# Performance work log

Measured on AMD Instinct MI355X. Metric: run time of the kernel, lower is better.

## Reference

```python
import jax, jax.numpy as jnp
import numpy as np

B = 8192         # graphs per batch
NPG = 39         # nodes per graph (from 4560 = 40*(105+9))
N = B * NPG      # total nodes
DEG = 8          # avg degree
E = N * DEG      # total edges
NEG_SLOPE = 0.2


def _glorot(key, shape):
    fan = sum(shape) if len(shape) > 1 else shape[0] + 1
    s = jnp.sqrt(6.0 / fan)
    return jax.random.uniform(key, shape, jnp.float32, -s, s)


def setup_inputs() -> dict:
    key = jax.random.key(0)
    ks = jax.random.split(key, 32)
    x = jax.random.normal(ks[0], (N, 1), jnp.float32)
    # edges constrained within each graph
    epg = NPG * DEG
    off = jnp.repeat(jnp.arange(B, dtype=jnp.int64) * NPG, epg)
    src = jax.random.randint(ks[1], (B * epg,), 0, NPG, jnp.int64) + off
    dst = jax.random.randint(ks[2], (B * epg,), 0, NPG, jnp.int64) + off
    edge_index = jnp.stack([src, dst], 0)
    batch_ids = jnp.repeat(jnp.arange(B, dtype=jnp.int64), NPG)
    dims = [(1, 8), (8, 64), (64, 32), (32, 9)]
    p = {}
    ki = 3
    for li, (fi, fo) in enumerate(dims, 1):
        p[f'W{li}'] = _glorot(ks[ki], (fi, fo)); ki += 1
        p[f'as{li}'] = _glorot(ks[ki], (fo,)); ki += 1
        p[f'ad{li}'] = _glorot(ks[ki], (fo,)); ki += 1
        p[f'b{li}'] = jnp.zeros((fo,), jnp.float32)
    p['lw1'] = _glorot(ks[ki], (4560, 1024)); ki += 1
    p['lb1'] = jnp.zeros((1024,), jnp.float32)
    p['lw2'] = _glorot(ks[ki], (1024, 128)); ki += 1
    p['lb2'] = jnp.zeros((128,), jnp.float32)
    p['lw3'] = _glorot(ks[ki], (128, 9)); ki += 1
    p['lb3'] = jnp.zeros((9,), jnp.float32)
    return {'x': x, 'edge_index': edge_index, 'batch_ids': batch_ids, **p}


def gat_layer(x, src, dst, W, a_s, a_d, b):
    # PyG GATConv, heads=1: h=xW; e_ij = LeakyReLU(a_s.h[src]+a_d.h[dst]);
    # softmax per destination node; out = sum_j alpha * h[src] + bias
    h = x @ W                                   # [N, Fo]
    s_n = h @ a_s                               # [N]
    d_n = h @ a_d                               # [N]
    e = jax.nn.leaky_relu(s_n[src] + d_n[dst], NEG_SLOPE)   # [E+N]
    m = jax.ops.segment_max(e, dst, num_segments=N)
    w = jnp.exp(e - m[dst])
    denom = jax.ops.segment_sum(w, dst, num_segments=N)
    alpha = w / (denom[dst] + 1e-16)
    out = jax.ops.segment_sum(h[src] * alpha[:, None], dst, num_segments=N)
    return out + b


def reference(x, edge_index, batch_ids, W1, as1, ad1, b1, W2, as2, ad2, b2,
              W3, as3, ad3, b3, W4, as4, ad4, b4, lw1, lb1, lw2, lb2, lw3, lb3):
    # add self-loops (PyG GATConv default)
    sl = jnp.arange(N, dtype=edge_index.dtype)
    src = jnp.concatenate([edge_index[0], sl])
    dst = jnp.concatenate([edge_index[1], sl])
    pool = lambda h: jax.ops.segment_max(h, batch_ids, num_segments=B)

    x0 = x.reshape(-1, 1)
    res = x0.reshape(B, -1)
    out0 = pool(x0)
    h1 = jax.nn.relu(gat_layer(x0, src, dst, W1, as1, ad1, b1))
    res1, out1 = h1.reshape(B, -1), pool(h1)
    h2 = jax.nn.relu(gat_layer(h1, src, dst, W2, as2, ad2, b2))
    res2, out2 = h2.reshape(B, -1), pool(h2)
    h3 = jax.nn.relu(gat_layer(h2, src, dst, W3, as3, ad3, b3))
    res3, out3 = h3.reshape(B, -1), pool(h3)
    h4 = jax.nn.relu(gat_layer(h3, src, dst, W4, as4, ad4, b4))
    res4, out4 = h4.reshape(B, -1), pool(h4)

    f = jnp.concatenate([res, res1, res2, res3, res4,
                         out0, out1, out2, out3, out4], axis=1)  # [B, 4560]
    f = jax.nn.relu(f @ lw1 + lb1)
    f = jax.nn.relu(f @ lw2 + lb2)
    return f @ lw3 + lb3
```

## Files before the change

kernel.cpp:

```cpp
#include <hip/hip_runtime.h>

#define NPG   39
#define NGRAPH 8192
#define EPG   312
#define EDG   351
#define E0    2555904
#define FDIM  4560
#define KP    4608

typedef __bf16 bf16x8 __attribute__((ext_vector_type(8)));
typedef float  f32x4  __attribute__((ext_vector_type(4)));

__device__ __forceinline__ unsigned short f2b(float f) {
  unsigned int u = __float_as_uint(f);
  u += 0x7fffu + ((u >> 16) & 1u);
  return (unsigned short)(u >> 16);
}
__device__ __forceinline__ unsigned int pk2(float lo, float hi) {
  return (unsigned int)f2b(lo) | ((unsigned int)f2b(hi) << 16);
}
__device__ __forceinline__ float b2f(unsigned short u) {
  return __uint_as_float((unsigned int)u << 16);
}
__device__ __forceinline__ void wsync() {
  asm volatile("s_waitcnt lgkmcnt(0)" ::: "memory");
}
__device__ __forceinline__ void gsync() {
  asm volatile("s_waitcnt vmcnt(0) lgkmcnt(0)" ::: "memory");
}

__shared__ alignas(16) unsigned short Htb[32 * 64];
__shared__ alignas(16) unsigned short alf16[40 * 64];
__shared__ float sn[40];
__shared__ float dn[48];
__shared__ unsigned char csr_src[EDG + 1];
__shared__ unsigned short csr_ptr[NPG + 1];

template<int Fi, int Fo, int KPAD, int KT1, int NT_STORE, int HALVES,
         int DT, int SCOL, int DCOL>
__device__ __forceinline__ void layerM(float x0,
                                       const unsigned short* __restrict__ Wb,
                                       const float* __restrict__ W1,
                                       const float* __restrict__ as1,
                                       const float* __restrict__ ad1,
                                       const float* __restrict__ bias,
                                       unsigned short* __restrict__ f_row,
                                       int in_off, int res_off, int out_off,
                                       int lane) {
  constexpr int NTH = NT_STORE / HALVES;
  constexpr int VW  = (HALVES == 2) ? 32 : Fo;
  constexpr bool SWZST = (VW == 32);
  const int r15 = lane & 15, g = lane >> 4;
  const f32x4 z = {0.f, 0.f, 0.f, 0.f};
  const uint4 z4 = {0u, 0u, 0u, 0u};
  unsigned short* stg = Htb;

#pragma unroll
  for (int i = 0; i < 5; ++i) *(uint4*)&alf16[lane * 8 + i * 512] = z4;

  if constexpr (Fi == 1) {
    float was = 0.f, wad = 0.f;
#pragma unroll
    for (int o = 0; o < 8; ++o) { float w = W1[o]; was += w * as1[o]; wad += w * ad1[o]; }
    if (lane < NPG) {
      sn[lane] = x0 * was; dn[lane] = x0 * wad;
#pragma unroll
      for (int o = 0; o < 8; ++o) {
        int idx = o * 64 + ((((lane >> 3) ^ (o & 7)) << 3)) + (lane & 7);
        Htb[idx] = f2b(x0 * W1[o]);
      }
    }
  } else {
    gsync();
    f32x4 cd[3];
#pragma unroll
    for (int mt = 0; mt < 3; ++mt) cd[mt] = z;
#pragma unroll
    for (int kt = 0; kt < KT1; ++kt) {
      bf16x8 aF[3];
#pragma unroll
      for (int mt = 0; mt < 3; ++mt) {
        int row = 16 * mt + r15;
        row = (row > 39) ? 39 : row;
        aF[mt] = *(const bf16x8*)&f_row[in_off + row * Fi + kt * 32 + g * 8];
      }
      bf16x8 bD = *(const bf16x8*)&Wb[(16 * DT + r15) * KPAD + kt * 32 + g * 8];
#pragma unroll
      for (int mt = 0; mt < 3; ++mt)
        cd[mt] = __builtin_amdgcn_mfma_f32_16x16x32_bf16(aF[mt], bD, cd[mt], 0, 0, 0);
    }
#pragma unroll
    for (int mt = 0; mt < 3; ++mt)
#pragma unroll
      for (int v = 0; v < 4; ++v) {
        float t = cd[mt][v] + __shfl_xor(cd[mt][v], 4);
        int r = 16 * mt + g * 4 + v;
        if (r15 == SCOL && r < NPG) sn[r] = t;
        if (r15 == DCOL && r < NPG) dn[r] = t;
      }
  }
  wsync();

  if (lane < NPG) {
    int rs = csr_ptr[lane], re = csr_ptr[lane + 1];
    float dv = dn[lane];
    float m = -3.4e38f;
    for (int k = rs; k < re; ++k) {
      float e = sn[csr_src[k]] + dv;
      e = (e >= 0.f) ? e : 0.2f * e;
      m = fmaxf(m, e);
    }
    float den = 0.f;
    for (int k = rs; k < re; ++k) {
      int s = csr_src[k];
      float e = sn[s] + dv;
      e = (e >= 0.f) ? e : 0.2f * e;
      float w = __expf(e - m);
      int idx = lane * 64 + ((((s >> 3) ^ (lane & 7)) << 3)) + (s & 7);
      float cur = b2f(alf16[idx]);
      unsigned short nb = f2b(cur + w);
      alf16[idx] = nb;
      den += b2f(nb) - cur;
    }
    dn[lane] = 1.f / (den + 1e-16f);
  }
  wsync();

  float invr[3][4];
#pragma unroll
  for (int mt = 0; mt < 3; ++mt)
#pragma unroll
    for (int v = 0; v < 4; ++v) invr[mt][v] = dn[16 * mt + g * 4 + v];

  float pool_[NT_STORE];
#pragma unroll
  for (int s = 0; s < NT_STORE; ++s) pool_[s] = 0.f;

#pragma unroll
  for (int h = 0; h < HALVES; ++h) {
    const int colbase = (HALVES == 2) ? 32 * h : 0;
    if constexpr (Fi > 1) {
      f32x4 c1[3][NTH];
#pragma unroll
      for (int mt = 0; mt < 3; ++mt)
#pragma unroll
        for (int tl = 0; tl < NTH; ++tl) c1[mt][tl] = z;
#pragma unroll
      for (int kt = 0; kt < KT1; ++kt) {
        bf16x8 aF[3];
#pragma unroll
        for (int mt = 0; mt < 3; ++mt) {
          int row = 16 * mt + r15;
          row = (row > 39) ? 39 : row;
          aF[mt] = *(const bf16x8*)&f_row[in_off + row * Fi + kt * 32 + g * 8];
        }
#pragma unroll
        for (int tl = 0; tl < NTH; ++tl) {
          int nt = h * NTH + tl;
          bf16x8 bW = *(const bf16x8*)&Wb[(16 * nt + r15) * KPAD + kt * 32 + g * 8];
#pragma unroll
          for (int mt = 0; mt < 3; ++mt)
            c1[mt][tl] = __builtin_amdgcn_mfma_f32_16x16x32_bf16(aF[mt], bW, c1[mt][tl], 0, 0, 0);
        }
      }
#pragma unroll
      for (int tl = 0; tl < NTH; ++tl) {
        int p = r15 + 16 * tl;
#pragma unroll
        for (int mt = 0; mt < 3; ++mt) {
          uint2 w;
          w.x = pk2(c1[mt][tl][0], c1[mt][tl][1]);
          w.y = pk2(c1[mt][tl][2], c1[mt][tl][3]);
          int idx = p * 64 + (((2 * mt + (g >> 1)) ^ (p & 7)) << 3) + (g & 1) * 4;
          *(uint2*)&Htb[idx] = w;
        }
      }
    }
    wsync();
    f32x4 c2[3][NTH];
#pragma unroll
    for (int mt = 0; mt < 3; ++mt)
#pragma unroll
      for (int tl = 0; tl < NTH; ++tl) c2[mt][tl] = z;
#pragma unroll
    for (int kt = 0; kt < 2; ++kt) {
      bf16x8 aA[3];
#pragma unroll
      for (int mt = 0; mt < 3; ++mt) {
        int row = 16 * mt + r15;
        aA[mt] = *(const bf16x8*)&alf16[row * 64 + ((((4 * kt + g) ^ (row & 7))) << 3)];
      }
#pragma unroll
      for (int tl = 0; tl < NTH; ++tl) {
        int p = r15 + 16 * tl;
        bf16x8 bH = *(const bf16x8*)&Htb[p * 64 + ((((4 * kt + g) ^ (p & 7))) << 3)];
#pragma unroll
        for (int mt = 0; mt < 3; ++mt)
          c2[mt][tl] = __builtin_amdgcn_mfma_f32_16x16x32_bf16(aA[mt], bH, c2[mt][tl], 0, 0, 0);
      }
    }
#pragma unroll
    for (int tl = 0; tl < NTH; ++tl) {
      int c = r15 + 16 * (h * NTH + tl);
      float bv = (c < Fo) ? bias[c] : 0.f;
#pragma unroll
      for (int mt = 0; mt < 3; ++mt)
#pragma unroll
        for (int v = 0; v < 4; ++v) {
          int r = 16 * mt + g * 4 + v;
          float val = fmaxf(c2[mt][tl][v] * invr[mt][v] + bv, 0.f);
          if (r < NPG && c < Fo) {
            int sc = c - colbase;
            int so = SWZST ? ((sc >> 3) ^ ((r >> 2) & 3)) : (sc >> 3);
            stg[r * VW + (so << 3) + (sc & 7)] = f2b(val);
            pool_[h * NTH + tl] = fmaxf(pool_[h * NTH + tl], val);
          }
        }
    }
    wsync();

    if constexpr (Fo == 9) {
      for (int j = lane; j < 43; j += 64)
        *(uint4*)&f_row[res_off + j * 8] = *(const uint4*)&stg[j * 8];
      if (lane < 7) f_row[res_off + 344 + lane] = stg[344 + lane];
    } else {
      constexpr int OPR = VW / 8;
      for (int j = lane; j < NPG * OPR; j += 64) {
        int r = (OPR == 4) ? (j >> 2) : j;
        int o = (OPR == 4) ? (j & 3) : 0;
        int so = SWZST ? (o ^ ((r >> 2) & 3)) : o;
        *(uint4*)&f_row[res_off + r * Fo + colbase + 8 * o] =
            *(const uint4*)&stg[r * VW + 8 * so];
      }
    }
    wsync();
  }

#pragma unroll
  for (int s = 0; s < NT_STORE; ++s) {
    float pv = pool_[s];
    pv = fmaxf(pv, __shfl_xor(pv, 16));
    pv = fmaxf(pv, __shfl_xor(pv, 32));
    int c = r15 + 16 * s;
    if (g == 0 && c < Fo) f_row[out_off + c] = f2b(pv);
  }
}

__global__ __launch_bounds__(64, 4) void gat_fused(
    const float* __restrict__ x, const int* __restrict__ ei,
    const float* __restrict__ W1, const float* __restrict__ as1, const float* __restrict__ ad1,
    const float* __restrict__ b1, const float* __restrict__ b2,
    const float* __restrict__ b3, const float* __restrict__ b4,
    const unsigned short* __restrict__ Wb,
    unsigned short* __restrict__ f) {
  const int b = blockIdx.x;
  const int lane = threadIdx.x;
  const int base = b * NPG;
  const int* srcg = ei + (size_t)b * EPG;
  const int* dstg = ei + E0 + (size_t)b * EPG;
  unsigned short* f_row = f + (size_t)b * KP;
  int* cnt = (int*)sn;
  const uint4 z4 = {0u, 0u, 0u, 0u};

#pragma unroll
  for (int i = 0; i < 4; ++i) *(uint4*)&Htb[lane * 8 + i * 512] = z4;

  float xv = 0.f;
  if (lane < NPG) {
    xv = x[(size_t)base + lane];
    f_row[lane] = f2b(xv);
  }
  if (lane == 0) f_row[39] = 0;
  if (lane < KP - 4561) f_row[4561 + lane] = 0;
  float mx = (lane < NPG) ? xv : -3.4e38f;
#pragma unroll
  for (int st = 1; st < 64; st <<= 1) { float t = __shfl_xor(mx, st); mx = fmaxf(mx, t); }
  if (lane == 0) f_row[4447] = f2b(mx);
  if (lane < NPG) cnt[lane] = 1;
  wsync();

  int es[5], ed[5];
#pragma unroll
  for (int it = 0; it < 5; ++it) {
    int e = lane + 64 * it;
    if (e < EPG) {
      int s = srcg[e] - base, d = dstg[e] - base;
      s = min(max(s, 0), NPG - 1);
      d = min(max(d, 0), NPG - 1);
      es[it] = s; ed[it] = d;
      atomicAdd(&cnt[d], 1);
    } else { es[it] = -1; ed[it] = 0; }
  }
  wsync();

  int c = (lane < NPG) ? cnt[lane] : 0;
  int v = c;
#pragma unroll
  for (int off = 1; off < 64; off <<= 1) { int t = __shfl_up(v, off); if (lane >= off) v += t; }
  int excl = v - c;
  if (lane < NPG) csr_ptr[lane] = (unsigned short)excl;
  if (lane == NPG - 1) csr_ptr[NPG] = (unsigned short)EDG;
  wsync();
  if (lane < NPG) cnt[lane] = excl;
  wsync();

  if (lane < NPG) { int p = atomicAdd(&cnt[lane], 1); csr_src[p] = (unsigned char)lane; }
#pragma unroll
  for (int it = 0; it < 5; ++it) {
    if (es[it] >= 0) {
      int p = atomicAdd(&cnt[ed[it]], 1);
      p = min(p, EDG - 1);
      csr_src[p] = (unsigned char)es[it];
    }
  }
  wsync();

  const unsigned short* Wb2 = Wb;
  const unsigned short* Wb3 = Wb + 2560;
  const unsigned short* Wb4 = Wb + 5632;

  layerM< 1,  8,  0,  0,  1,  1,  0,  0,  0>(xv, nullptr, W1, as1, ad1, b1, f_row, 0,    40,   4448, lane);
  layerM< 8, 64, 32,  1,  4,  2,  4,  0,  1>(0.f, Wb2, nullptr, nullptr, nullptr, b2, f_row, 40,   352,  4456, lane);
  layerM<64, 32, 64,  2,  2,  1,  2,  0,  1>(0.f, Wb3, nullptr, nullptr, nullptr, b3, f_row, 352,  2848, 4520, lane);
  layerM<32,  9, 32,  1,  1,  1,  0, 10, 11>(0.f, Wb4, nullptr, nullptr, nullptr, b4, f_row, 2848, 4096, 4552, lane);
}

__global__ __launch_bounds__(256) void prep_wb(
    const float* __restrict__ W2, const float* __restrict__ as2, const float* __restrict__ ad2,
    const float* __restrict__ W3, const float* __restrict__ as3, const float* __restrict__ ad3,
    const float* __restrict__ W4, const float* __restrict__ as4, const float* __restrict__ ad4,
    unsigned short* __restrict__ Wb) {
  const int tid = threadIdx.x;
  for (int i = tid; i < 80 * 32; i += 256) {
    int o = i >> 5, k = i & 31; float v = 0.f;
    if (k < 8) {
      if (o < 64) v = W2[k * 64 + o];
      else if (o == 64 || o == 68) { float s = 0; for (int j = 0; j < 64; ++j) s += W2[k * 64 + j] * as2[j];
        float hi = b2f(f2b(s)); v = (o == 64) ? hi : (s - hi); }
      else if (o == 65 || o == 69) { float s = 0; for (int j = 0; j < 64; ++j) s += W2[k * 64 + j] * ad2[j];
        float hi = b2f(f2b(s)); v = (o == 65) ? hi : (s - hi); }
    }
    Wb[i] = f2b(v);
  }
  for (int i = tid; i < 48 * 64; i += 256) {
    int o = i >> 6, k = i & 63; float v = 0.f;
    if (o < 32) v = W3[k * 32 + o];
    else if (o == 32 || o == 36) { float s = 0; for (int j = 0; j < 32; ++j) s += W3[k * 32 + j] * as3[j];
      float hi = b2f(f2b(s)); v = (o == 32) ? hi : (s - hi); }
    else if (o == 33 || o == 37) { float s = 0; for (int j = 0; j < 32; ++j) s += W3[k * 32 + j] * ad3[j];
      float hi = b2f(f2b(s)); v = (o == 33) ? hi : (s - hi); }
    Wb[2560 + i] = f2b(v);
  }
  for (int i = tid; i < 16 * 32; i += 256) {
    int o = i >> 5, k = i & 31; float v = 0.f;
    if (o < 9) v = W4[k * 9 + o];
    else if (o == 10 || o == 14) { float s = 0; for (int j = 0; j < 9; ++j) s += W4[k * 9 + j] * as4[j];
      float hi = b2f(f2b(s)); v = (o == 10) ? hi : (s - hi); }
    else if (o == 11 || o == 15) { float s = 0; for (int j = 0; j < 9; ++j) s += W4[k * 9 + j] * ad4[j];
      float hi = b2f(f2b(s)); v = (o == 11) ? hi : (s - hi); }
    Wb[5632 + i] = f2b(v);
  }
}

template<bool PERM>
__global__ __launch_bounds__(256) void tcast(const float* __restrict__ in,
                                             unsigned short* __restrict__ out,
                                             int K, int NN, int Kpad) {
  __shared__ float tile[64 * 65];
  const int k0 = blockIdx.x * 64, n0 = blockIdx.y * 64;
  const int tid = threadIdx.x;
#pragma unroll
  for (int i = 0; i < 16; ++i) {
    int idx = i * 256 + tid;
    int r = idx >> 6, c = idx & 63;
    int k = k0 + r;
    int ko;
    if constexpr (PERM) {
      ko = (k < 39) ? k : ((k == 39 || k > FDIM) ? -1 : k - 1);
    } else {
      ko = (k < K) ? k : -1;
    }
    tile[r * 65 + c] = (ko >= 0) ? in[(size_t)ko * NN + n0 + c] : 0.f;
  }
  __syncthreads();
#pragma unroll
  for (int i = 0; i < 16; ++i) {
    int idx = i * 256 + tid;
    int r = idx >> 6, c = idx & 63;
    out[(size_t)(n0 + r) * Kpad + k0 + c] = f2b(tile[c * 65 + r]);
  }
}

template<bool OUT_BF16>
__global__ __launch_bounds__(256) void mfma_gemm(const unsigned short* __restrict__ A,
    const unsigned short* __restrict__ Bt, unsigned short* __restrict__ Cb,
    float* __restrict__ Cf, const float* __restrict__ bias, int K, int N, int gridN) {
  __shared__ alignas(16) unsigned short As[128 * 64];
  __shared__ alignas(16) unsigned short Bs[128 * 64];
  const int tid = threadIdx.x;
  const int lane = tid & 63;
  const int wave = tid >> 6;
  const int wy = wave >> 1, wx = wave & 1;

  const int wg = blockIdx.x;
  const int xcd = wg & 7, idx = wg >> 3;
  const int mpr = (int)(gridDim.x >> 3) / gridN;
  const int m_local = idx / gridN;
  const int n = idx - m_local * gridN;
  const int m0 = (xcd * mpr + m_local) * 128;
  const int n0 = n * 128;

  f32x4 acc[4][4];
  const f32x4 z = {0.f, 0.f, 0.f, 0.f};
#pragma unroll
  for (int i = 0; i < 4; ++i)
#pragma unroll
    for (int j = 0; j < 4; ++j) acc[i][j] = z;

  const int srow = lane >> 3;
  const int sch  = (lane & 7) ^ srow;
  const int q    = lane >> 4;
  const int rm   = lane & 15;

  for (int k0 = 0; k0 < K; k0 += 64) {
    __syncthreads();
#pragma unroll
    for (int t = 0; t < 4; ++t) {
      int r0 = wave * 32 + t * 8;
      const unsigned short* ga = A  + (size_t)(m0 + r0 + srow) * K + k0 + sch * 8;
      const unsigned short* gb = Bt + (size_t)(n0 + r0 + srow) * K + k0 + sch * 8;
      __builtin_amdgcn_global_load_lds(
          (const __attribute__((address_space(1))) unsigned int*)(const void*)ga,
          (__attribute__((address_space(3))) unsigned int*)(void*)&As[r0 * 64], 16, 0, 0);
      __builtin_amdgcn_global_load_lds(
          (const __attribute__((address_space(1))) unsigned int*)(const void*)gb,
          (__attribute__((address_space(3))) unsigned int*)(void*)&Bs[r0 * 64], 16, 0, 0);
    }
    __syncthreads();
#pragma unroll
    for (int kk = 0; kk < 2; ++kk) {
      bf16x8 af[4], bfr[4];
#pragma unroll
      for (int i = 0; i < 4; ++i) {
        int ra = wy * 64 + i * 16 + rm;
        int rb = wx * 64 + i * 16 + rm;
        af[i]  = *(const bf16x8*)&As[ra * 64 + (((kk * 4 + q) ^ (ra & 7)) << 3)];
        bfr[i] = *(const bf16x8*)&Bs[rb * 64 + (((kk * 4 + q) ^ (rb & 7)) << 3)];
      }
#pragma unroll
      for (int i = 0; i < 4; ++i)
#pragma unroll
        for (int j = 0; j < 4; ++j)
          acc[i][j] = __builtin_amdgcn_mfma_f32_16x16x32_bf16(af[i], bfr[j], acc[i][j], 0, 0, 0);
    }
  }
  const int q4 = (lane >> 4) * 4;
#pragma unroll
  for (int i = 0; i < 4; ++i) {
#pragma unroll
    for (int j = 0; j < 4; ++j) {
      int row = m0 + wy * 64 + i * 16 + q4;
      int col = n0 + wx * 64 + j * 16 + rm;
      float bv = bias[col];
#pragma unroll
      for (int v = 0; v < 4; ++v) {
        float val = fmaxf(acc[i][j][v] + bv, 0.f);
        if constexpr (OUT_BF16) Cb[(size_t)(row + v) * N + col] = f2b(val);
        else                    Cf[(size_t)(row + v) * N + col] = val;
      }
    }
  }
}

__global__ __launch_bounds__(256) void mlp3(const float* __restrict__ g2,
                                            const float* __restrict__ w3,
                                            const float* __restrict__ b3,
                                            float* __restrict__ out) {
  __shared__ float gs[64 * 130];
  __shared__ float ws3[128 * 9];
  const int r0 = blockIdx.x * 64;
  const int tid = threadIdx.x;
  for (int i = tid; i < 64 * 128; i += 256)
    gs[(i >> 7) * 130 + (i & 127)] = g2[(size_t)r0 * 128 + i];
  for (int i = tid; i < 128 * 9; i += 256) ws3[i] = w3[i];
  __syncthreads();
  for (int idx = tid; idx < 64 * 9; idx += 256) {
    int r = idx / 9, c = idx - r * 9;
    float acc = b3[c];
#pragma unroll 8
    for (int k = 0; k < 128; ++k) acc += gs[r * 130 + k] * ws3[k * 9 + c];
    out[(size_t)(r0 + r) * 9 + c] = acc;
  }
}

extern "C" void kernel_launch(void* const* d_in, const int* in_sizes, int n_in,
                              void* d_out, int out_size, void* d_ws, size_t ws_size,
                              hipStream_t stream) {
  const float* x   = (const float*)d_in[0];
  const int*   ei  = (const int*)d_in[1];
  const float* W1  = (const float*)d_in[3];
  const float* as1 = (const float*)d_in[4];
  const float* ad1 = (const float*)d_in[5];
  const float* b1  = (const float*)d_in[6];
  const float* W2  = (const float*)d_in[7];
  const float* as2 = (const float*)d_in[8];
  const float* ad2 = (const float*)d_in[9];
  const float* b2  = (const float*)d_in[10];
  const float* W3  = (const float*)d_in[11];
  const float* as3 = (const float*)d_in[12];
  const float* ad3 = (const float*)d_in[13];
  const float* b3  = (const float*)d_in[14];
  const float* W4  = (const float*)d_in[15];
  const float* as4 = (const float*)d_in[16];
  const float* ad4 = (const float*)d_in[17];
  const float* b4  = (const float*)d_in[18];
  const float* lw1 = (const float*)d_in[19];
  const float* lb1 = (const float*)d_in[20];
  const float* lw2 = (const float*)d_in[21];
  const float* lb2 = (const float*)d_in[22];
  const float* lw3 = (const float*)d_in[23];
  const float* lb3 = (const float*)d_in[24];
  float* out = (float*)d_out;

  unsigned short* f   = (unsigned short*)d_ws;
  unsigned short* w1t = f   + (size_t)NGRAPH * KP;
  unsigned short* w2t = w1t + (size_t)1024 * KP;
  unsigned short* g1  = w2t + (size_t)128 * 1024;
  float*          g2  = (float*)(g1 + (size_t)NGRAPH * 1024);
  unsigned short* Wb  = g1;

  prep_wb<<<1, 256, 0, stream>>>(W2, as2, ad2, W3, as3, ad3, W4, as4, ad4, Wb);
  tcast<true ><<<dim3(KP / 64, 1024 / 64), 256, 0, stream>>>(lw1, w1t, FDIM, 1024, KP);
  tcast<false><<<dim3(1024 / 64, 128 / 64), 256, 0, stream>>>(lw2, w2t, 1024, 128, 1024);

  gat_fused<<<NGRAPH, 64, 0, stream>>>(x, ei, W1, as1, ad1,
      b1, b2, b3, b4, Wb, f);

  mfma_gemm<true ><<<512, 256, 0, stream>>>(
      f, w1t, g1, nullptr, lb1, KP, 1024, 8);
  mfma_gemm<false><<<64, 256, 0, stream>>>(
      g1, w2t, nullptr, g2, lb2, 1024, 128, 1);

  mlp3<<<NGRAPH / 64, 256, 0, stream>>>(g2, lw3, lb3, out);
}
```

Measured before the change: 222.4 us.

## Double-buffer LDS tiles in MFMA GEMM to overlap loads with compute

The GEMM k-loop now keeps two LDS buffers for the A and B tiles. It issues the async global-to-LDS loads for the next k-tile before computing on the current one, and uses explicit vmcnt waits and raw barriers in place of __syncthreads. This is meant to hide global load latency behind MFMA work. In exchange it doubles LDS use to 64KB per block, which may reduce occupancy. Correctness also depends on the hand-written vmcnt count matching the eight loads issued per stage.

```diff
diff --git a/kernel.cpp b/kernel.cpp
--- a/kernel.cpp
+++ b/kernel.cpp
@@ -395,8 +395,8 @@
 __global__ __launch_bounds__(256) void mfma_gemm(const unsigned short* __restrict__ A,
     const unsigned short* __restrict__ Bt, unsigned short* __restrict__ Cb,
     float* __restrict__ Cf, const float* __restrict__ bias, int K, int N, int gridN) {
-  __shared__ alignas(16) unsigned short As[128 * 64];
-  __shared__ alignas(16) unsigned short Bs[128 * 64];
+  __shared__ alignas(16) unsigned short As[2][128 * 64];
+  __shared__ alignas(16) unsigned short Bs[2][128 * 64];
   const int tid = threadIdx.x;
   const int lane = tid & 63;
   const int wave = tid >> 6;
@@ -422,21 +422,34 @@
   const int q    = lane >> 4;
   const int rm   = lane & 15;
 
+#define STAGE(buf, kk0)                                                              \
+  {                                                                                  \
+    _Pragma("unroll")                                                                \
+    for (int t = 0; t < 4; ++t) {                                                    \
+      int r0 = wave * 32 + t * 8;                                                    \
+      const unsigned short* ga = A  + (size_t)(m0 + r0 + srow) * K + (kk0) + sch * 8;\
+      const unsigned short* gb = Bt + (size_t)(n0 + r0 + srow) * K + (kk0) + sch * 8;\
+      __builtin_amdgcn_global_load_lds(                                              \
+          (const __attribute__((address_space(1))) unsigned int*)(const void*)ga,    \
+          (__attribute__((address_space(3))) unsigned int*)(void*)&As[buf][r0 * 64], \
+          16, 0, 0);                                                                 \
+      __builtin_amdgcn_global_load_lds(                                              \
+          (const __attribute__((address_space(1))) unsigned int*)(const void*)gb,    \
+          (__attribute__((address_space(3))) unsigned int*)(void*)&Bs[buf][r0 * 64], \
+          16, 0, 0);                                                                 \
+    }                                                                                \
+  }
+
+  STAGE(0, 0);
+  int cur = 0;
   for (int k0 = 0; k0 < K; k0 += 64) {
-    __syncthreads();
-#pragma unroll
-    for (int t = 0; t < 4; ++t) {
-      int r0 = wave * 32 + t * 8;
-      const unsigned short* ga = A  + (size_t)(m0 + r0 + srow) * K + k0 + sch * 8;
-      const unsigned short* gb = Bt + (size_t)(n0 + r0 + srow) * K + k0 + sch * 8;
-      __builtin_amdgcn_global_load_lds(
-          (const __attribute__((address_space(1))) unsigned int*)(const void*)ga,
-          (__attribute__((address_space(3))) unsigned int*)(void*)&As[r0 * 64], 16, 0, 0);
-      __builtin_amdgcn_global_load_lds(
-          (const __attribute__((address_space(1))) unsigned int*)(const void*)gb,
-          (__attribute__((address_space(3))) unsigned int*)(void*)&Bs[r0 * 64], 16, 0, 0);
-    }
-    __syncthreads();
+    if (k0 + 64 < K) {
+      STAGE(cur ^ 1, k0 + 64);
+      asm volatile("s_waitcnt vmcnt(8)" ::: "memory");
+    } else {
+      asm volatile("s_waitcnt vmcnt(0)" ::: "memory");
+    }
+    __builtin_amdgcn_s_barrier();
 #pragma unroll
     for (int kk = 0; kk < 2; ++kk) {
       bf16x8 af[4], bfr[4];
@@ -444,8 +457,8 @@
       for (int i = 0; i < 4; ++i) {
         int ra = wy * 64 + i * 16 + rm;
         int rb = wx * 64 + i * 16 + rm;
-        af[i]  = *(const bf16x8*)&As[ra * 64 + (((kk * 4 + q) ^ (ra & 7)) << 3)];
-        bfr[i] = *(const bf16x8*)&Bs[rb * 64 + (((kk * 4 + q) ^ (rb & 7)) << 3)];
+        af[i]  = *(const bf16x8*)&As[cur][ra * 64 + (((kk * 4 + q) ^ (ra & 7)) << 3)];
+        bfr[i] = *(const bf16x8*)&Bs[cur][rb * 64 + (((kk * 4 + q) ^ (rb & 7)) << 3)];
       }
 #pragma unroll
       for (int i = 0; i < 4; ++i)
@@ -453,7 +466,11 @@
         for (int j = 0; j < 4; ++j)
           acc[i][j] = __builtin_amdgcn_mfma_f32_16x16x32_bf16(af[i], bfr[j], acc[i][j], 0, 0, 0);
     }
-  }
+    __builtin_amdgcn_s_barrier();
+    cur ^= 1;
+  }
+#undef STAGE
+
   const int q4 = (lane >> 4) * 4;
 #pragma unroll
   for (int i = 0; i < 4; ++i) {
```

Result: faster. 211.8 us (-4.7%).
